# Performance work log

Hardware: AMD Instinct MI355X
Metric: run time of the kernel (lower is better)

The kernel has to match this reference:

```python
import jax, jax.numpy as jnp
import numpy as np

NUM_HEADS = 16


def setup_inputs() -> dict:
    key = jax.random.key(0)
    ks = jax.random.split(key, 9)
    B, N, D = 2, 2048, 1024
    w = 0.02
    return {
        "x": jax.random.normal(ks[0], (B, N, D), dtype=jnp.float32),
        "wq": jax.random.normal(ks[1], (D, D), dtype=jnp.float32) * w,
        "bq": jax.random.normal(ks[2], (D,), dtype=jnp.float32) * w,
        "wk": jax.random.normal(ks[3], (D, D), dtype=jnp.float32) * w,
        "bk": jax.random.normal(ks[4], (D,), dtype=jnp.float32) * w,
        "wv": jax.random.normal(ks[5], (D, D), dtype=jnp.float32) * w,
        "bv": jax.random.normal(ks[6], (D,), dtype=jnp.float32) * w,
        "wo": jax.random.normal(ks[7], (D, D), dtype=jnp.float32) * w,
        "bo": jax.random.normal(ks[8], (D,), dtype=jnp.float32) * w,
    }


def _heads(t, B, N, H, hd):
    # (B, N, D) -> (B, H, N, hd)
    return t.reshape(B, N, H, hd).transpose(0, 2, 1, 3)


def reference(x, wq, bq, wk, bk, wv, bv, wo, bo):
    B, N, D = x.shape
    H = NUM_HEADS
    hd = D // H
    q = _heads(x @ wq.T + bq, B, N, H, hd)
    k = _heads(x @ wk.T + bk, B, N, H, hd)
    v = _heads(x @ wv.T + bv, B, N, H, hd)
    # pairwise L2 distances via GEMM expansion: ||q-k||^2 = |q|^2 + |k|^2 - 2 q.k
    q2 = jnp.sum(q * q, axis=-1)                      # (B, H, N)
    k2 = jnp.sum(k * k, axis=-1)                      # (B, H, N)
    qk = jnp.einsum('bhid,bhjd->bhij', q, k)          # (B, H, N, N)
    d2 = jnp.maximum(q2[..., :, None] + k2[..., None, :] - 2.0 * qk, 1e-12)
    attn = jax.nn.softmax(-jnp.sqrt(d2), axis=-1)     # (B, H, N, N)
    out = jnp.einsum('bhij,bhjd->bhid', attn, v)      # (B, H, N, hd)
    out = out.transpose(0, 2, 1, 3).reshape(B, N, D)
    return out @ wo.T + bo
```

## Files before the change

kernel.cpp:

```cpp
#include <hip/hip_runtime.h>


typedef __attribute__((ext_vector_type(8))) short sh8;
typedef __attribute__((ext_vector_type(4))) short sh4;
typedef __attribute__((ext_vector_type(4))) float f4;

#define QK_SCALE 1.44269504f
#define D2_CLAMP 2.0814e-12f

__device__ __forceinline__ float bf2f(short s) {
  union { unsigned u; float f; } c;
  c.u = ((unsigned)(unsigned short)s) << 16;
  return c.f;
}
__device__ __forceinline__ short f2bf(float f) {
  union { float f; unsigned u; } c;
  c.f = f;
  return (short)((c.u + 0x8000u) >> 16);
}
__device__ __forceinline__ sh8 pack8(f4 a, f4 b) {
  sh8 r;
  r[0] = f2bf(a[0]); r[1] = f2bf(a[1]); r[2] = f2bf(a[2]); r[3] = f2bf(a[3]);
  r[4] = f2bf(b[0]); r[5] = f2bf(b[1]); r[6] = f2bf(b[2]); r[7] = f2bf(b[3]);
  return r;
}
__device__ __forceinline__ float exp2neg(float x) {
  return __builtin_amdgcn_exp2f(-x);
}

#define GLDS16(g, l)                                                      \
  __builtin_amdgcn_global_load_lds(                                       \
      (__attribute__((address_space(1))) void*)(void*)(g),                \
      (__attribute__((address_space(3))) void*)(void*)(l), 16, 0, 0)

__global__ __launch_bounds__(256) void cvt_bf16(const float* __restrict__ src,
                                                short* __restrict__ dst, int n) {
  const int i = (blockIdx.x * 256 + threadIdx.x) * 8;
  if (i < n)
    *(sh8*)(dst + i) = pack8(*(const f4*)(src + i), *(const f4*)(src + i + 4));
}

__global__ __launch_bounds__(256) void cvt_w4(
    const float* __restrict__ wq, const float* __restrict__ wk,
    const float* __restrict__ wv, const float* __restrict__ wo,
    short* __restrict__ dst) {
  const float* srcs[4] = {wq, wk, wv, wo};
  const float* s = srcs[blockIdx.y];
  short* d = dst + (size_t)blockIdx.y * 1048576;
  const int i = (blockIdx.x * 256 + threadIdx.x) * 8;
  *(sh8*)(d + i) = pack8(*(const f4*)(s + i), *(const f4*)(s + i + 4));
}

__global__ __launch_bounds__(256) void gemm_qkvp(
    const float* __restrict__ X, const float* __restrict__ Wq,
    const float* __restrict__ Bq, const float* __restrict__ Wk,
    const float* __restrict__ Bk, const float* __restrict__ Wv,
    const float* __restrict__ Bv, short* __restrict__ Qp,
    short* __restrict__ Kp, short* __restrict__ Vtp, int w0, int nblkP) {
  __shared__ short As[128 * 32];
  __shared__ short Bs[128 * 32];
  const int t = threadIdx.x;
  const int wave = t >> 6;
  const int lane = t & 63;
  const int l15 = lane & 15;
  const int quad = lane >> 4;
  const int m0 = blockIdx.y * 128;
  const int which = blockIdx.x / nblkP;
  const int n0l = (blockIdx.x % nblkP) * 128;
  const int wrow0 = w0 + n0l;
  const float* W = (which == 0) ? Wq : ((which == 1) ? Wk : Wv);
  const float* Bias = (which == 0) ? Bq : ((which == 1) ? Bk : Bv);
  const float qkscl = (which == 2) ? 1.0f : QK_SCALE;
  const int wm = (wave & 1) * 64;
  const int wn = (wave >> 1) * 64;

  f4 acc[4][4];
#pragma unroll
  for (int i = 0; i < 4; ++i)
#pragma unroll
    for (int j = 0; j < 4; ++j) acc[i][j] = (f4){0.f, 0.f, 0.f, 0.f};

  const float* ag = X + (size_t)(m0 + (t >> 2)) * 1024 + (t & 3) * 8;
  const float* bg = W + (size_t)(wrow0 + (t >> 2)) * 1024 + (t & 3) * 8;

  for (int kt = 0; kt < 1024; kt += 32) {
    const sh8 a0 = pack8(*(const f4*)(ag + kt), *(const f4*)(ag + kt + 4));
    const sh8 a1 =
        pack8(*(const f4*)(ag + 65536 + kt), *(const f4*)(ag + 65536 + kt + 4));
    const sh8 b0 = pack8(*(const f4*)(bg + kt), *(const f4*)(bg + kt + 4));
    const sh8 b1 =
        pack8(*(const f4*)(bg + 65536 + kt), *(const f4*)(bg + 65536 + kt + 4));
    __syncthreads();
    *(sh8*)(As + t * 8) = a0;
    *(sh8*)(As + 2048 + t * 8) = a1;
    *(sh8*)(Bs + t * 8) = b0;
    *(sh8*)(Bs + 2048 + t * 8) = b1;
    __syncthreads();
    sh8 af[4], bf[4];
#pragma unroll
    for (int i = 0; i < 4; ++i) {
      af[i] = *(const sh8*)(As + (wm + i * 16 + l15) * 32 + quad * 8);
      bf[i] = *(const sh8*)(Bs + (wn + i * 16 + l15) * 32 + quad * 8);
    }
#pragma unroll
    for (int i = 0; i < 4; ++i)
#pragma unroll
      for (int j = 0; j < 4; ++j)
        acc[i][j] =
            __builtin_amdgcn_mfma_f32_16x16x32_bf16(af[i], bf[j], acc[i][j], 0, 0, 0);
  }

#pragma unroll
  for (int j = 0; j < 4; ++j) {
    const int ngl = n0l + wn + j * 16 + l15;
    const float bias = Bias[w0 + ngl];
    const int hl = ngl >> 6;
    const int d = ngl & 63;
#pragma unroll
    for (int i = 0; i < 4; ++i) {
#pragma unroll
      for (int r = 0; r < 4; ++r) {
        const int m = m0 + wm + i * 16 + quad * 4 + r;
        const int slot = (m >> 11) * 16 + hl;
        const int mm = m & 2047;
        const short o = f2bf((acc[i][j][r] + bias) * qkscl);
        if (which == 0)
          Qp[((size_t)slot * 2048 + mm) * 64 + d] = o;
        else if (which == 1)
          Kp[((size_t)slot * 2048 + mm) * 64 + d] = o;
        else
          Vtp[((size_t)slot * 64 + d) * 2048 + mm] = o;
      }
    }
  }
}

__global__ __launch_bounds__(256) void gemm_qkv_bf(
    const short* __restrict__ X, const short* __restrict__ Wq,
    const float* __restrict__ Bq, const short* __restrict__ Wk,
    const float* __restrict__ Bk, const short* __restrict__ Wv,
    const float* __restrict__ Bv, short* __restrict__ Qp,
    short* __restrict__ Kp, short* __restrict__ Vtp) {
  __shared__ short As[128 * 32];
  __shared__ short Bs[128 * 32];
  const int t = threadIdx.x;
  const int wave = t >> 6;
  const int lane = t & 63;
  const int l15 = lane & 15;
  const int quad = lane >> 4;
  const int m0 = blockIdx.y * 128;
  const int which = blockIdx.x >> 3;
  const int n0l = (blockIdx.x & 7) * 128;
  const short* W = (which == 0) ? Wq : ((which == 1) ? Wk : Wv);
  const float* Bias = (which == 0) ? Bq : ((which == 1) ? Bk : Bv);
  const float qkscl = (which == 2) ? 1.0f : QK_SCALE;
  const int wm = (wave & 1) * 64;
  const int wn = (wave >> 1) * 64;

  f4 acc[4][4];
#pragma unroll
  for (int i = 0; i < 4; ++i)
#pragma unroll
    for (int j = 0; j < 4; ++j) acc[i][j] = (f4){0.f, 0.f, 0.f, 0.f};

  const short* ag = X + (size_t)(m0 + (t >> 2)) * 1024 + (t & 3) * 8;
  const short* bg = W + (size_t)(n0l + (t >> 2)) * 1024 + (t & 3) * 8;
  short* al = As + wave * 512;
  short* bl = Bs + wave * 512;

  for (int kt = 0; kt < 1024; kt += 32) {
    __syncthreads();
    GLDS16(ag + kt, al);
    GLDS16(ag + 65536 + kt, al + 2048);
    GLDS16(bg + kt, bl);
    GLDS16(bg + 65536 + kt, bl + 2048);
    __syncthreads();
    sh8 af[4], bf[4];
#pragma unroll
    for (int i = 0; i < 4; ++i) {
      af[i] = *(const sh8*)(As + (wm + i * 16 + l15) * 32 + quad * 8);
      bf[i] = *(const sh8*)(Bs + (wn + i * 16 + l15) * 32 + quad * 8);
    }
#pragma unroll
    for (int i = 0; i < 4; ++i)
#pragma unroll
      for (int j = 0; j < 4; ++j)
        acc[i][j] =
            __builtin_amdgcn_mfma_f32_16x16x32_bf16(af[i], bf[j], acc[i][j], 0, 0, 0);
  }

#pragma unroll
  for (int j = 0; j < 4; ++j) {
    const int ngl = n0l + wn + j * 16 + l15;
    const float bias = Bias[ngl];
    const int hl = ngl >> 6;
    const int d = ngl & 63;
#pragma unroll
    for (int i = 0; i < 4; ++i) {
#pragma unroll
      for (int r = 0; r < 4; ++r) {
        const int m = m0 + wm + i * 16 + quad * 4 + r;
        const int slot = (m >> 11) * 16 + hl;
        const int mm = m & 2047;
        const short o = f2bf((acc[i][j][r] + bias) * qkscl);
        if (which == 0)
          Qp[((size_t)slot * 2048 + mm) * 64 + d] = o;
        else if (which == 1)
          Kp[((size_t)slot * 2048 + mm) * 64 + d] = o;
        else
          Vtp[((size_t)slot * 64 + d) * 2048 + mm] = o;
      }
    }
  }
}

__global__ __launch_bounds__(256) void sumsq(const short* __restrict__ Qp,
                                             const short* __restrict__ Kp,
                                             float* __restrict__ q2a,
                                             float* __restrict__ k2a, int R) {
  const int tid = blockIdx.x * 256 + threadIdx.x;
  const bool isQ = tid < R;
  const int r = isQ ? tid : tid - R;
  const short* p = (isQ ? Qp : Kp) + (size_t)r * 64;
  float s = 0.f;
#pragma unroll
  for (int i = 0; i < 8; ++i) {
    sh8 v = *(const sh8*)(p + i * 8);
#pragma unroll
    for (int j = 0; j < 8; ++j) {
      float f = bf2f(v[j]);
      s = fmaf(f, f, s);
    }
  }
  (isQ ? q2a : k2a)[r] = s;
}

__global__ __launch_bounds__(512, 2) void attn4(
    const short* __restrict__ Qp, const short* __restrict__ Kp,
    const short* __restrict__ Vtp, const float* __restrict__ q2a,
    const float* __restrict__ k2a, short* __restrict__ attH) {
  __shared__ short Ks[128 * 72];
  __shared__ short Vs[64 * 136];
  const int t = threadIdx.x;
  const int wave = t >> 6;
  const int lane = t & 63;
  const int l15 = lane & 15;
  const int quad = lane >> 4;
  const int hy = blockIdx.y;
  const int qt = blockIdx.x;
  const int bz = blockIdx.z;
  const size_t hb = (size_t)bz * gridDim.y + hy;
  const size_t base = hb * 2048;
  const int qrowA = qt * 256 + wave * 32 + l15;
  const int qrowB = qrowA + 16;

  const short* qpA = Qp + (base + qrowA) * 64 + quad * 8;
  const sh8 qA0 = *(const sh8*)qpA;
  const sh8 qA1 = *(const sh8*)(qpA + 32);
  const short* qpB = Qp + (base + qrowB) * 64 + quad * 8;
  const sh8 qB0 = *(const sh8*)qpB;
  const sh8 qB1 = *(const sh8*)(qpB + 32);
  const float q2A = q2a[base + qrowA];
  const float q2B = q2a[base + qrowB];

  float lA = 0.f, lB = 0.f;
  f4 oA0 = (f4){0.f, 0.f, 0.f, 0.f}, oA1 = oA0, oA2 = oA0, oA3 = oA0;
  f4 oB0 = oA0, oB1 = oA0, oB2 = oA0, oB3 = oA0;

  const float* k2p = k2a + base + quad * 4;

  const short* kg0 = Kp + (base + (t >> 3)) * 64 + (t & 7) * 8;
  const short* vg0 = Vtp + (hb * 64 + (t >> 4)) * 2048 + (t & 15) * 8;
  sh8 kv0 = *(const sh8*)kg0;
  sh8 kv1 = *(const sh8*)(kg0 + 64 * 64);
  sh8 vv0 = *(const sh8*)vg0;
  sh8 vv1 = *(const sh8*)(vg0 + 32 * 2048);

  for (int k0 = 0; k0 < 2048; k0 += 128) {
    __syncthreads();
    *(sh8*)(Ks + (t >> 3) * 72 + (t & 7) * 8) = kv0;
    *(sh8*)(Ks + (64 + (t >> 3)) * 72 + (t & 7) * 8) = kv1;
    *(sh8*)(Vs + (t >> 4) * 136 + (t & 15) * 8) = vv0;
    *(sh8*)(Vs + (32 + (t >> 4)) * 136 + (t & 15) * 8) = vv1;
    __syncthreads();
    if (k0 + 128 < 2048) {
      kv0 = *(const sh8*)(kg0 + (size_t)(k0 + 128) * 64);
      kv1 = *(const sh8*)(kg0 + (size_t)(k0 + 128) * 64 + 64 * 64);
      vv0 = *(const sh8*)(vg0 + k0 + 128);
      vv1 = *(const sh8*)(vg0 + 32 * 2048 + k0 + 128);
    }

#pragma unroll
    for (int sub = 0; sub < 8; ++sub) {
      const int j = sub * 16;
      const sh8 kf0 = *(const sh8*)(Ks + (j + l15) * 72 + quad * 8);
      const sh8 kf1 = *(const sh8*)(Ks + (j + l15) * 72 + 32 + quad * 8);
      f4 stA = (f4){0.f, 0.f, 0.f, 0.f};
      f4 stB = (f4){0.f, 0.f, 0.f, 0.f};
      stA = __builtin_amdgcn_mfma_f32_16x16x32_bf16(kf0, qA0, stA, 0, 0, 0);
      stA = __builtin_amdgcn_mfma_f32_16x16x32_bf16(kf1, qA1, stA, 0, 0, 0);
      stB = __builtin_amdgcn_mfma_f32_16x16x32_bf16(kf0, qB0, stB, 0, 0, 0);
      stB = __builtin_amdgcn_mfma_f32_16x16x32_bf16(kf1, qB1, stB, 0, 0, 0);
      const f4 k2v = *(const f4*)(k2p + k0 + j);
      float pA[4], pB[4];
#pragma unroll
      for (int r = 0; r < 4; ++r) {
        const float dA = fmaxf(fmaf(-2.f, stA[r], q2A + k2v[r]), D2_CLAMP);
        pA[r] = exp2neg(__builtin_amdgcn_sqrtf(dA));
        const float dB = fmaxf(fmaf(-2.f, stB[r], q2B + k2v[r]), D2_CLAMP);
        pB[r] = exp2neg(__builtin_amdgcn_sqrtf(dB));
      }
      lA += (pA[0] + pA[1]) + (pA[2] + pA[3]);
      lB += (pB[0] + pB[1]) + (pB[2] + pB[3]);
      sh4 pfA, pfB;
#pragma unroll
      for (int r = 0; r < 4; ++r) {
        pfA[r] = f2bf(pA[r]);
        pfB[r] = f2bf(pB[r]);
      }
      const sh4 vf0 = *(const sh4*)(Vs + l15 * 136 + j + quad * 4);
      const sh4 vf1 = *(const sh4*)(Vs + (l15 + 16) * 136 + j + quad * 4);
      const sh4 vf2 = *(const sh4*)(Vs + (l15 + 32) * 136 + j + quad * 4);
      const sh4 vf3 = *(const sh4*)(Vs + (l15 + 48) * 136 + j + quad * 4);
      oA0 = __builtin_amdgcn_mfma_f32_16x16x16bf16_1k(pfA, vf0, oA0, 0, 0, 0);
      oA1 = __builtin_amdgcn_mfma_f32_16x16x16bf16_1k(pfA, vf1, oA1, 0, 0, 0);
      oA2 = __builtin_amdgcn_mfma_f32_16x16x16bf16_1k(pfA, vf2, oA2, 0, 0, 0);
      oA3 = __builtin_amdgcn_mfma_f32_16x16x16bf16_1k(pfA, vf3, oA3, 0, 0, 0);
      oB0 = __builtin_amdgcn_mfma_f32_16x16x16bf16_1k(pfB, vf0, oB0, 0, 0, 0);
      oB1 = __builtin_amdgcn_mfma_f32_16x16x16bf16_1k(pfB, vf1, oB1, 0, 0, 0);
      oB2 = __builtin_amdgcn_mfma_f32_16x16x16bf16_1k(pfB, vf2, oB2, 0, 0, 0);
      oB3 = __builtin_amdgcn_mfma_f32_16x16x16bf16_1k(pfB, vf3, oB3, 0, 0, 0);
    }
  }

  lA += __shfl_xor(lA, 16);
  lA += __shfl_xor(lA, 32);
  lB += __shfl_xor(lB, 16);
  lB += __shfl_xor(lB, 32);
  float ilA[4], ilB[4];
#pragma unroll
  for (int r = 0; r < 4; ++r) {
    ilA[r] = 1.f / __shfl(lA, quad * 4 + r);
    ilB[r] = 1.f / __shfl(lB, quad * 4 + r);
  }

  const int rbA = qt * 256 + wave * 32 + quad * 4;
  const size_t offA = ((size_t)bz * 2048 + rbA) * 1024 + hy * 64 + l15;
  const size_t offB = offA + (size_t)16 * 1024;
  const f4* ocA[4] = {&oA0, &oA1, &oA2, &oA3};
  const f4* ocB[4] = {&oB0, &oB1, &oB2, &oB3};
#pragma unroll
  for (int c = 0; c < 4; ++c)
#pragma unroll
    for (int r = 0; r < 4; ++r) {
      attH[offA + (size_t)r * 1024 + c * 16] = f2bf((*ocA[c])[r] * ilA[r]);
      attH[offB + (size_t)r * 1024 + c * 16] = f2bf((*ocB[c])[r] * ilB[r]);
    }
}

__global__ __launch_bounds__(256) void attn_c(
    const short* __restrict__ Qp, const short* __restrict__ Kp,
    const short* __restrict__ Vtp, const float* __restrict__ q2a,
    const float* __restrict__ k2a, float* __restrict__ attF, int col0) {
  const int t = threadIdx.x;
  const int wave = t >> 6;
  const int lane = t & 63;
  const int l15 = lane & 15;
  const int quad = lane >> 4;
  const int hy = blockIdx.y;
  const int qt = blockIdx.x;
  const size_t base = (size_t)hy * 2048;
  const int qrow = qt * 64 + wave * 16 + l15;

  const short* qp = Qp + (base + qrow) * 64 + quad * 8;
  const sh8 qf0 = *(const sh8*)qp;
  const sh8 qf1 = *(const sh8*)(qp + 32);
  const float q2 = q2a[base + qrow];

  float l_run = 0.f;
  f4 o0 = (f4){0.f, 0.f, 0.f, 0.f}, o1 = o0, o2 = o0, o3 = o0;

  const short* kbase = Kp + (base + l15) * 64 + quad * 8;
  const float* k2p = k2a + base + quad * 4;
  const short* vbase = Vtp + ((size_t)hy * 64 + l15) * 2048 + quad * 4;

  for (int j = 0; j < 2048; j += 16) {
    const sh8 kf0 = *(const sh8*)(kbase + (size_t)j * 64);
    const sh8 kf1 = *(const sh8*)(kbase + (size_t)j * 64 + 32);
    f4 st = (f4){0.f, 0.f, 0.f, 0.f};
    st = __builtin_amdgcn_mfma_f32_16x16x32_bf16(kf0, qf0, st, 0, 0, 0);
    st = __builtin_amdgcn_mfma_f32_16x16x32_bf16(kf1, qf1, st, 0, 0, 0);
    const f4 k2v = *(const f4*)(k2p + j);
    float p[4];
#pragma unroll
    for (int r = 0; r < 4; ++r) {
      const float d2 = fmaxf(fmaf(-2.f, st[r], q2 + k2v[r]), D2_CLAMP);
      p[r] = exp2neg(__builtin_amdgcn_sqrtf(d2));
    }
    l_run += (p[0] + p[1]) + (p[2] + p[3]);
    sh4 pf;
#pragma unroll
    for (int r = 0; r < 4; ++r) pf[r] = f2bf(p[r]);
    const sh4 vf0 = *(const sh4*)(vbase + j);
    const sh4 vf1 = *(const sh4*)(vbase + 16 * 2048 + j);
    const sh4 vf2 = *(const sh4*)(vbase + 32 * 2048 + j);
    const sh4 vf3 = *(const sh4*)(vbase + 48 * 2048 + j);
    o0 = __builtin_amdgcn_mfma_f32_16x16x16bf16_1k(pf, vf0, o0, 0, 0, 0);
    o1 = __builtin_amdgcn_mfma_f32_16x16x16bf16_1k(pf, vf1, o1, 0, 0, 0);
    o2 = __builtin_amdgcn_mfma_f32_16x16x16bf16_1k(pf, vf2, o2, 0, 0, 0);
    o3 = __builtin_amdgcn_mfma_f32_16x16x16bf16_1k(pf, vf3, o3, 0, 0, 0);
  }

  l_run += __shfl_xor(l_run, 16);
  l_run += __shfl_xor(l_run, 32);
  const float il0 = 1.f / __shfl(l_run, quad * 4 + 0);
  const float il1 = 1.f / __shfl(l_run, quad * 4 + 1);
  const float il2 = 1.f / __shfl(l_run, quad * 4 + 2);
  const float il3 = 1.f / __shfl(l_run, quad * 4 + 3);

  const int rowbase = qt * 64 + wave * 16 + quad * 4;
  const f4* oc[4] = {&o0, &o1, &o2, &o3};
  const float il[4] = {il0, il1, il2, il3};
  const size_t off0 = (size_t)rowbase * 1024 + col0 + hy * 64 + l15;
#pragma unroll
  for (int c = 0; c < 4; ++c)
#pragma unroll
    for (int r = 0; r < 4; ++r)
      attF[off0 + (size_t)r * 1024 + c * 16] = (*oc[c])[r] * il[r];
}

__global__ __launch_bounds__(256) void gemm_out_bf64(
    const short* __restrict__ A, const short* __restrict__ W,
    const float* __restrict__ Bias, float* __restrict__ Out) {
  __shared__ short As[64 * 32];
  __shared__ short Bs[128 * 32];
  const int t = threadIdx.x;
  const int wave = t >> 6;
  const int lane = t & 63;
  const int l15 = lane & 15;
  const int quad = lane >> 4;
  const int m0 = blockIdx.y * 64;
  const int n0 = blockIdx.x * 128;
  const int wm = (wave & 1) * 32;
  const int wn = (wave >> 1) * 64;

  f4 acc[2][4];
#pragma unroll
  for (int i = 0; i < 2; ++i)
#pragma unroll
    for (int j = 0; j < 4; ++j) acc[i][j] = (f4){0.f, 0.f, 0.f, 0.f};

  const short* ag = A + (size_t)(m0 + (t >> 2)) * 1024 + (t & 3) * 8;
  const short* bg = W + (size_t)(n0 + (t >> 2)) * 1024 + (t & 3) * 8;
  short* al = As + wave * 512;
  short* bl = Bs + wave * 512;

  for (int kt = 0; kt < 1024; kt += 32) {
    __syncthreads();
    GLDS16(ag + kt, al);
    GLDS16(bg + kt, bl);
    GLDS16(bg + 65536 + kt, bl + 2048);
    __syncthreads();
    sh8 af[2], bf[4];
#pragma unroll
    for (int i = 0; i < 2; ++i)
      af[i] = *(const sh8*)(As + (wm + i * 16 + l15) * 32 + quad * 8);
#pragma unroll
    for (int j = 0; j < 4; ++j)
      bf[j] = *(const sh8*)(Bs + (wn + j * 16 + l15) * 32 + quad * 8);
#pragma unroll
    for (int i = 0; i < 2; ++i)
#pragma unroll
      for (int j = 0; j < 4; ++j)
        acc[i][j] =
            __builtin_amdgcn_mfma_f32_16x16x32_bf16(af[i], bf[j], acc[i][j], 0, 0, 0);
  }

#pragma unroll
  for (int j = 0; j < 4; ++j) {
    const int n = n0 + wn + j * 16 + l15;
    const float bias = Bias[n];
#pragma unroll
    for (int i = 0; i < 2; ++i) {
#pragma unroll
      for (int r = 0; r < 4; ++r) {
        const int m = m0 + wm + i * 16 + quad * 4 + r;
        Out[(size_t)m * 1024 + n] = acc[i][j][r] + bias;
      }
    }
  }
}

__global__ __launch_bounds__(256) void gemm_out_ws64(
    const short* __restrict__ A, const float* __restrict__ W,
    const float* __restrict__ Bias, float* __restrict__ Out) {
  __shared__ short As[64 * 32];
  __shared__ short Bs[128 * 32];
  const int t = threadIdx.x;
  const int wave = t >> 6;
  const int lane = t & 63;
  const int l15 = lane & 15;
  const int quad = lane >> 4;
  const int m0 = blockIdx.y * 64;
  const int n0 = blockIdx.x * 128;
  const int wm = (wave & 1) * 32;
  const int wn = (wave >> 1) * 64;

  f4 acc[2][4];
#pragma unroll
  for (int i = 0; i < 2; ++i)
#pragma unroll
    for (int j = 0; j < 4; ++j) acc[i][j] = (f4){0.f, 0.f, 0.f, 0.f};

  const short* ag = A + (size_t)(m0 + (t >> 2)) * 1024 + (t & 3) * 8;
  const float* bg = W + (size_t)(n0 + (t >> 2)) * 1024 + (t & 3) * 8;
  short* al = As + wave * 512;

  for (int kt = 0; kt < 1024; kt += 32) {
    const sh8 b0 = pack8(*(const f4*)(bg + kt), *(const f4*)(bg + kt + 4));
    const sh8 b1 =
        pack8(*(const f4*)(bg + 65536 + kt), *(const f4*)(bg + 65536 + kt + 4));
    __syncthreads();
    GLDS16(ag + kt, al);
    *(sh8*)(Bs + t * 8) = b0;
    *(sh8*)(Bs + 2048 + t * 8) = b1;
    __syncthreads();
    sh8 af[2], bf[4];
#pragma unroll
    for (int i = 0; i < 2; ++i)
      af[i] = *(const sh8*)(As + (wm + i * 16 + l15) * 32 + quad * 8);
#pragma unroll
    for (int j = 0; j < 4; ++j)
      bf[j] = *(const sh8*)(Bs + (wn + j * 16 + l15) * 32 + quad * 8);
#pragma unroll
    for (int i = 0; i < 2; ++i)
#pragma unroll
      for (int j = 0; j < 4; ++j)
        acc[i][j] =
            __builtin_amdgcn_mfma_f32_16x16x32_bf16(af[i], bf[j], acc[i][j], 0, 0, 0);
  }

#pragma unroll
  for (int j = 0; j < 4; ++j) {
    const int n = n0 + wn + j * 16 + l15;
    const float bias = Bias[n];
#pragma unroll
    for (int i = 0; i < 2; ++i) {
#pragma unroll
      for (int r = 0; r < 4; ++r) {
        const int m = m0 + wm + i * 16 + quad * 4 + r;
        Out[(size_t)m * 1024 + n] = acc[i][j][r] + bias;
      }
    }
  }
}

__global__ __launch_bounds__(256) void outproj_inplace(
    float* __restrict__ AO, const float* __restrict__ W,
    const float* __restrict__ Bias) {
  __shared__ short attS[16 * 264];
  const int t = threadIdx.x;
  const int wave = t >> 6;
  const int lane = t & 63;
  const int l15 = lane & 15;
  const int quad = lane >> 4;
  const int m0 = blockIdx.x * 16;
  const int n0w = wave * 256;

  f4 acc[16];
#pragma unroll
  for (int i = 0; i < 16; ++i) acc[i] = (f4){0.f, 0.f, 0.f, 0.f};

  for (int kc = 0; kc < 4; ++kc) {
    __syncthreads();
#pragma unroll
    for (int i = 0; i < 2; ++i) {
      const int e = i * 2048 + t * 8;
      const int row = e >> 8;
      const int col = e & 255;
      const float* src = AO + (size_t)(m0 + row) * 1024 + kc * 256 + col;
      *(sh8*)(attS + row * 264 + col) =
          pack8(*(const f4*)src, *(const f4*)(src + 4));
    }
    __syncthreads();
    for (int ktl = 0; ktl < 256; ktl += 32) {
      const sh8 af = *(const sh8*)(attS + l15 * 264 + ktl + quad * 8);
      const int kt = kc * 256 + ktl;
#pragma unroll
      for (int nf = 0; nf < 16; ++nf) {
        const float* wp = W + (size_t)(n0w + nf * 16 + l15) * 1024 + kt + quad * 8;
        const sh8 bf = pack8(*(const f4*)wp, *(const f4*)(wp + 4));
        acc[nf] = __builtin_amdgcn_mfma_f32_16x16x32_bf16(af, bf, acc[nf], 0, 0, 0);
      }
    }
  }
  __syncthreads();

#pragma unroll
  for (int nf = 0; nf < 16; ++nf) {
    const int n = n0w + nf * 16 + l15;
    const float bias = Bias[n];
#pragma unroll
    for (int r = 0; r < 4; ++r) {
      const int m = m0 + quad * 4 + r;
      AO[(size_t)m * 1024 + n] = acc[nf][r] + bias;
    }
  }
}

extern "C" void kernel_launch(void* const* d_in, const int* in_sizes, int n_in,
                              void* d_out, int out_size, void* d_ws,
                              size_t ws_size, hipStream_t stream) {
  const float* x = (const float*)d_in[0];
  const float* wq = (const float*)d_in[1];
  const float* bq = (const float*)d_in[2];
  const float* wk = (const float*)d_in[3];
  const float* bk = (const float*)d_in[4];
  const float* wv = (const float*)d_in[5];
  const float* bv = (const float*)d_in[6];
  const float* wo = (const float*)d_in[7];
  const float* bo = (const float*)d_in[8];
  float* out = (float*)d_out;

  const size_t NEED_A2 = 50855936ULL;
  const size_t NEED_A = 34078720ULL;

  if (ws_size >= NEED_A) {
    short* Qp = (short*)d_ws;
    short* Kp = Qp + 4194304;
    short* Vtp = Kp + 4194304;
    short* attAll = Vtp + 4194304;
    float* q2 = (float*)(attAll + 4194304);
    float* k2 = q2 + 65536;

    if (ws_size >= NEED_A2) {
      short* Xb = (short*)(k2 + 65536);
      short* Wqb = Xb + 4194304;
      cvt_bf16<<<2048, 256, 0, stream>>>(x, Xb, 4194304);
      cvt_w4<<<dim3(512, 4), 256, 0, stream>>>(wq, wk, wv, wo, Wqb);
      gemm_qkv_bf<<<dim3(24, 32), 256, 0, stream>>>(
          Xb, Wqb, bq, Wqb + 1048576, bk, Wqb + 2097152, bv, Qp, Kp, Vtp);
      sumsq<<<512, 256, 0, stream>>>(Qp, Kp, q2, k2, 65536);
      attn4<<<dim3(8, 16, 2), 512, 0, stream>>>(Qp, Kp, Vtp, q2, k2, attAll);
      gemm_out_bf64<<<dim3(8, 64), 256, 0, stream>>>(attAll, Wqb + 3145728,
                                                     bo, out);
    } else {
      gemm_qkvp<<<dim3(24, 32), 256, 0, stream>>>(x, wq, bq, wk, bk, wv, bv,
                                                  Qp, Kp, Vtp, 0, 8);
      sumsq<<<512, 256, 0, stream>>>(Qp, Kp, q2, k2, 65536);
      attn4<<<dim3(8, 16, 2), 512, 0, stream>>>(Qp, Kp, Vtp, q2, k2, attAll);
      gemm_out_ws64<<<dim3(8, 64), 256, 0, stream>>>(attAll, wo, bo, out);
    }
  } else {
    int G = 16;
    while (G > 2 && (size_t)G * 802816ULL > ws_size) G >>= 1;
    short* Qp = (short*)d_ws;
    short* Kp = Qp + (size_t)G * 131072;
    short* Vtp = Kp + (size_t)G * 131072;
    float* q2 = (float*)(Vtp + (size_t)G * 131072);
    float* k2 = q2 + (size_t)G * 2048;

    const int groups = 16 / G;
    for (int b = 0; b < 2; ++b) {
      const float* xb = x + (size_t)b * 2097152;
      float* attB = out + (size_t)b * 2097152;
      for (int g = 0; g < groups; ++g) {
        gemm_qkvp<<<dim3(3 * (G / 2), 16), 256, 0, stream>>>(
            xb, wq, bq, wk, bk, wv, bv, Qp, Kp, Vtp, g * G * 64, G / 2);
        sumsq<<<16 * G, 256, 0, stream>>>(Qp, Kp, q2, k2, G * 2048);
        attn_c<<<dim3(32, G), 256, 0, stream>>>(Qp, Kp, Vtp, q2, k2, attB,
                                                g * G * 64);
      }
    }
    outproj_inplace<<<256, 256, 0, stream>>>(out, wo, bo);
  }
}
```

Measured before the change: 232.7 us.

## Shrink attention blocks to 256 threads and XOR-swizzle K/V shared tiles

Each attention block now has 256 threads covering 128 query rows instead of 512 threads covering 256, so the grid doubles to 512 blocks for better CU fill. The padded shared K/V tiles are replaced by unpadded tiles with an XOR column swizzle to avoid bank conflicts and cut LDS use, and each thread now loads four K and four V vectors per tile. The distance clamp becomes fabsf, saving an instruction per element, though tiny negative rounding errors now map to their magnitude instead of the clamp value. Halving the block size means each K/V tile is loaded and staged by twice as many blocks, so global and LDS traffic per query goes up.

Measured after the change: 229.7 us. Within noise of the previous version (-1.3%).

```diff
diff --git a/kernel.cpp b/kernel.cpp
--- a/kernel.cpp
+++ b/kernel.cpp
@@ -235,12 +235,12 @@
   (isQ ? q2a : k2a)[r] = s;
 }
 
-__global__ __launch_bounds__(512, 2) void attn4(
+__global__ __launch_bounds__(256, 2) void attn5(
     const short* __restrict__ Qp, const short* __restrict__ Kp,
     const short* __restrict__ Vtp, const float* __restrict__ q2a,
     const float* __restrict__ k2a, short* __restrict__ attH) {
-  __shared__ short Ks[128 * 72];
-  __shared__ short Vs[64 * 136];
+  __shared__ short Ks[128 * 64];
+  __shared__ short Vs[64 * 128];
   const int t = threadIdx.x;
   const int wave = t >> 6;
   const int lane = t & 63;
@@ -251,7 +251,7 @@
   const int bz = blockIdx.z;
   const size_t hb = (size_t)bz * gridDim.y + hy;
   const size_t base = hb * 2048;
-  const int qrowA = qt * 256 + wave * 32 + l15;
+  const int qrowA = qt * 128 + wave * 32 + l15;
   const int qrowB = qrowA + 16;
 
   const short* qpA = Qp + (base + qrowA) * 64 + quad * 8;
@@ -269,32 +269,53 @@
 
   const float* k2p = k2a + base + quad * 4;
 
-  const short* kg0 = Kp + (base + (t >> 3)) * 64 + (t & 7) * 8;
-  const short* vg0 = Vtp + (hb * 64 + (t >> 4)) * 2048 + (t & 15) * 8;
-  sh8 kv0 = *(const sh8*)kg0;
-  sh8 kv1 = *(const sh8*)(kg0 + 64 * 64);
-  sh8 vv0 = *(const sh8*)vg0;
-  sh8 vv1 = *(const sh8*)(vg0 + 32 * 2048);
+  const int kr = t >> 3, kc = t & 7;
+  const int vr = t >> 4, vc = t & 15;
+  const short* kg0 = Kp + (base + kr) * 64 + kc * 8;
+  const short* vg0 = Vtp + (hb * 64 + vr) * 2048 + vc * 8;
+  const int kidx = kr * 64 + ((kc ^ (kr & 7)) * 8);
+  const int vidx = vr * 128 + ((vc ^ (vr & 7)) * 8);
+
+  sh8 kp0 = *(const sh8*)kg0;
+  sh8 kp1 = *(const sh8*)(kg0 + 32 * 64);
+  sh8 kp2 = *(const sh8*)(kg0 + 64 * 64);
+  sh8 kp3 = *(const sh8*)(kg0 + 96 * 64);
+  sh8 vp0 = *(const sh8*)vg0;
+  sh8 vp1 = *(const sh8*)(vg0 + 16 * 2048);
+  sh8 vp2 = *(const sh8*)(vg0 + 32 * 2048);
+  sh8 vp3 = *(const sh8*)(vg0 + 48 * 2048);
 
   for (int k0 = 0; k0 < 2048; k0 += 128) {
     __syncthreads();
-    *(sh8*)(Ks + (t >> 3) * 72 + (t & 7) * 8) = kv0;
-    *(sh8*)(Ks + (64 + (t >> 3)) * 72 + (t & 7) * 8) = kv1;
-    *(sh8*)(Vs + (t >> 4) * 136 + (t & 15) * 8) = vv0;
-    *(sh8*)(Vs + (32 + (t >> 4)) * 136 + (t & 15) * 8) = vv1;
+    *(sh8*)(Ks + kidx) = kp0;
+    *(sh8*)(Ks + 32 * 64 + kidx) = kp1;
+    *(sh8*)(Ks + 64 * 64 + kidx) = kp2;
+    *(sh8*)(Ks + 96 * 64 + kidx) = kp3;
+    *(sh8*)(Vs + vidx) = vp0;
+    *(sh8*)(Vs + 16 * 128 + vidx) = vp1;
+    *(sh8*)(Vs + 32 * 128 + vidx) = vp2;
+    *(sh8*)(Vs + 48 * 128 + vidx) = vp3;
     __syncthreads();
     if (k0 + 128 < 2048) {
-      kv0 = *(const sh8*)(kg0 + (size_t)(k0 + 128) * 64);
-      kv1 = *(const sh8*)(kg0 + (size_t)(k0 + 128) * 64 + 64 * 64);
-      vv0 = *(const sh8*)(vg0 + k0 + 128);
-      vv1 = *(const sh8*)(vg0 + 32 * 2048 + k0 + 128);
+      const short* kg = kg0 + (size_t)(k0 + 128) * 64;
+      kp0 = *(const sh8*)kg;
+      kp1 = *(const sh8*)(kg + 32 * 64);
+      kp2 = *(const sh8*)(kg + 64 * 64);
+      kp3 = *(const sh8*)(kg + 96 * 64);
+      const short* vg = vg0 + k0 + 128;
+      vp0 = *(const sh8*)vg;
+      vp1 = *(const sh8*)(vg + 16 * 2048);
+      vp2 = *(const sh8*)(vg + 32 * 2048);
+      vp3 = *(const sh8*)(vg + 48 * 2048);
     }
 
 #pragma unroll
     for (int sub = 0; sub < 8; ++sub) {
       const int j = sub * 16;
-      const sh8 kf0 = *(const sh8*)(Ks + (j + l15) * 72 + quad * 8);
-      const sh8 kf1 = *(const sh8*)(Ks + (j + l15) * 72 + 32 + quad * 8);
+      const int krow = j + l15;
+      const int kcs = (quad ^ (krow & 7)) * 8;
+      const sh8 kf0 = *(const sh8*)(Ks + krow * 64 + kcs);
+      const sh8 kf1 = *(const sh8*)(Ks + krow * 64 + (kcs ^ 32));
       f4 stA = (f4){0.f, 0.f, 0.f, 0.f};
       f4 stB = (f4){0.f, 0.f, 0.f, 0.f};
       stA = __builtin_amdgcn_mfma_f32_16x16x32_bf16(kf0, qA0, stA, 0, 0, 0);
@@ -305,10 +326,10 @@
       float pA[4], pB[4];
 #pragma unroll
       for (int r = 0; r < 4; ++r) {
-        const float dA = fmaxf(fmaf(-2.f, stA[r], q2A + k2v[r]), D2_CLAMP);
-        pA[r] = exp2neg(__builtin_amdgcn_sqrtf(dA));
-        const float dB = fmaxf(fmaf(-2.f, stB[r], q2B + k2v[r]), D2_CLAMP);
-        pB[r] = exp2neg(__builtin_amdgcn_sqrtf(dB));
+        const float dA = fmaf(-2.f, stA[r], q2A + k2v[r]);
+        pA[r] = exp2neg(__builtin_amdgcn_sqrtf(fabsf(dA)));
+        const float dB = fmaf(-2.f, stB[r], q2B + k2v[r]);
+        pB[r] = exp2neg(__builtin_amdgcn_sqrtf(fabsf(dB)));
       }
       lA += (pA[0] + pA[1]) + (pA[2] + pA[3]);
       lB += (pB[0] + pB[1]) + (pB[2] + pB[3]);
@@ -318,10 +339,11 @@
         pfA[r] = f2bf(pA[r]);
         pfB[r] = f2bf(pB[r]);
       }
-      const sh4 vf0 = *(const sh4*)(Vs + l15 * 136 + j + quad * 4);
-      const sh4 vf1 = *(const sh4*)(Vs + (l15 + 16) * 136 + j + quad * 4);
-      const sh4 vf2 = *(const sh4*)(Vs + (l15 + 32) * 136 + j + quad * 4);
-      const sh4 vf3 = *(const sh4*)(Vs + (l15 + 48) * 136 + j + quad * 4);
+      const int vcol = ((sub * 2 + (quad >> 1)) ^ (l15 & 7)) * 8 + (quad & 1) * 4;
+      const sh4 vf0 = *(const sh4*)(Vs + l15 * 128 + vcol);
+      const sh4 vf1 = *(const sh4*)(Vs + (l15 + 16) * 128 + vcol);
+      const sh4 vf2 = *(const sh4*)(Vs + (l15 + 32) * 128 + vcol);
+      const sh4 vf3 = *(const sh4*)(Vs + (l15 + 48) * 128 + vcol);
       oA0 = __builtin_amdgcn_mfma_f32_16x16x16bf16_1k(pfA, vf0, oA0, 0, 0, 0);
       oA1 = __builtin_amdgcn_mfma_f32_16x16x16bf16_1k(pfA, vf1, oA1, 0, 0, 0);
       oA2 = __builtin_amdgcn_mfma_f32_16x16x16bf16_1k(pfA, vf2, oA2, 0, 0, 0);
@@ -344,7 +366,7 @@
     ilB[r] = 1.f / __shfl(lB, quad * 4 + r);
   }
 
-  const int rbA = qt * 256 + wave * 32 + quad * 4;
+  const int rbA = qt * 128 + wave * 32 + quad * 4;
   const size_t offA = ((size_t)bz * 2048 + rbA) * 1024 + hy * 64 + l15;
   const size_t offB = offA + (size_t)16 * 1024;
   const f4* ocA[4] = {&oA0, &oA1, &oA2, &oA3};
@@ -641,14 +663,14 @@
       gemm_qkv_bf<<<dim3(24, 32), 256, 0, stream>>>(
           Xb, Wqb, bq, Wqb + 1048576, bk, Wqb + 2097152, bv, Qp, Kp, Vtp);
       sumsq<<<512, 256, 0, stream>>>(Qp, Kp, q2, k2, 65536);
-      attn4<<<dim3(8, 16, 2), 512, 0, stream>>>(Qp, Kp, Vtp, q2, k2, attAll);
+      attn5<<<dim3(16, 16, 2), 256, 0, stream>>>(Qp, Kp, Vtp, q2, k2, attAll);
       gemm_out_bf64<<<dim3(8, 64), 256, 0, stream>>>(attAll, Wqb + 3145728,
                                                      bo, out);
     } else {
       gemm_qkvp<<<dim3(24, 32), 256, 0, stream>>>(x, wq, bq, wk, bk, wv, bv,
                                                   Qp, Kp, Vtp, 0, 8);
       sumsq<<<512, 256, 0, stream>>>(Qp, Kp, q2, k2, 65536);
-      attn4<<<dim3(8, 16, 2), 512, 0, stream>>>(Qp, Kp, Vtp, q2, k2, attAll);
+      attn5<<<dim3(16, 16, 2), 256, 0, stream>>>(Qp, Kp, Vtp, q2, k2, attAll);
       gemm_out_ws64<<<dim3(8, 64), 256, 0, stream>>>(attAll, wo, bo, out);
     }
   } else {
```
